# Kernel tuning notes

Hardware: AMD Instinct MI355X
Metric: run time of the kernel (lower is better)

## Reference

```python
import jax, jax.numpy as jnp
import numpy as np

B, N, K = 4, 4096, 10   # batch, num points, ED_nsample
SA, ED = 128, 4          # SA_conv_out, ED_conv_out


def _bn_pack(key, C):
    # rows: gamma, beta, running_mean, running_var (eval-mode BatchNorm1d)
    kg, kb, km, kv = jax.random.split(key, 4)
    g = 1.0 + 0.1 * jax.random.normal(kg, (C,))
    b = 0.1 * jax.random.normal(kb, (C,))
    m = 0.1 * jax.random.normal(km, (C,))
    v = jax.random.uniform(kv, (C,), minval=0.5, maxval=1.5)
    return jnp.stack([g, b, m, v])


def _conv_params(key, o, c):
    kw, kb = jax.random.split(key)
    return (jax.random.normal(kw, (o, c)) * (1.0 / np.sqrt(c)),
            0.01 * jax.random.normal(kb, (o,)))


def setup_inputs() -> dict:
    key = jax.random.key(0)
    ks = iter(jax.random.split(key, 32))
    inp = {}
    inp['pointcloud'] = jax.random.normal(next(ks), (B, N, 3), dtype=jnp.float32)
    inp['h1'] = jax.random.normal(next(ks), (B, SA, N), dtype=jnp.float32)      # Pointnet_Backbone output
    inp['h2'] = jax.random.normal(next(ks), (B, 1024, N), dtype=jnp.float32)    # DGCNN output
    shapes = {'dg1': (256, 1024), 'dg2': (64, 256), 'dg3': (32, 64),
              'c1': (512, 160), 'c2': (256, 512), 'c3': (128, 256), 'f': (128, 132)}
    for name, (o, c) in shapes.items():
        W, b = _conv_params(next(ks), o, c)
        inp['W_' + name], inp['b_' + name] = W, b
        inp['bn_' + name] = _bn_pack(next(ks), o)
    inp['W_ed1'] = jax.random.normal(next(ks), (ED, 3)) * 0.5
    inp['b_ed1'] = 0.01 * jax.random.normal(next(ks), (ED,))
    inp['W_ed2'] = jax.random.normal(next(ks), (ED, ED)) * 0.5
    inp['b_ed2'] = 0.01 * jax.random.normal(next(ks), (ED,))
    inp['numpoints'] = N
    return inp


def _bn1d(x, p, eps=1e-5):
    # x: [B, C, N]; p rows: gamma, beta, mean, var
    g, b, m, v = p
    inv = g * jax.lax.rsqrt(v + eps)
    return x * inv[:, None] + (b - m * inv)[:, None]


def _conv1(x, W, b):
    # 1x1 Conv1d == channel matmul. x: [B,C,N], W: [O,C]
    return jnp.einsum('oc,bcn->bon', W, x) + b[:, None]


def reference(pointcloud, h1, h2,
              W_dg1, b_dg1, bn_dg1, W_dg2, b_dg2, bn_dg2, W_dg3, b_dg3, bn_dg3,
              W_c1, b_c1, bn_c1, W_c2, b_c2, bn_c2, W_c3, b_c3, bn_c3,
              W_f, b_f, bn_f, W_ed1, b_ed1, W_ed2, b_ed2, numpoints):
    relu = jax.nn.relu
    xyz = pointcloud[..., :3]  # [B,N,3]

    # DGCNN feature reduction: 1024 -> 256 -> 64 -> 32
    h2_ = relu(_bn1d(_conv1(h2, W_dg1, b_dg1), bn_dg1))
    h2_ = relu(_bn1d(_conv1(h2_, W_dg2, b_dg2), bn_dg2))
    h2_ = relu(_bn1d(_conv1(h2_, W_dg3, b_dg3), bn_dg3))

    # fused feature: 160 -> 512 -> 256 -> 128
    f = jnp.concatenate([h1, h2_], axis=1)
    f_ = relu(_bn1d(_conv1(f, W_c1, b_c1), bn_c1))
    f_ = relu(_bn1d(_conv1(f_, W_c2, b_c2), bn_c2))
    f_ = relu(_bn1d(_conv1(f_, W_c3, b_c3), bn_c3))

    # knn_point: K nearest neighbors of each point within its cloud
    sq = jnp.sum(xyz * xyz, axis=-1)  # [B,N]
    d = sq[:, :, None] + sq[:, None, :] - 2.0 * jnp.einsum('bnd,bmd->bnm', xyz, xyz)
    _, idx = jax.lax.top_k(-d, K)  # [B,N,K]
    nbr = jax.vmap(lambda p, i: p[i])(xyz, idx)  # [B,N,K,3]

    # per-point 3x3 covariance + eigenvalues
    c = nbr - jnp.mean(nbr, axis=2, keepdims=True)
    cov = jnp.einsum('bnki,bnkj->bnij', c, c) / K  # [B,N,3,3]
    ev = jnp.linalg.eigvalsh(cov)  # [B,N,3] ascending

    # sub3_ED: Linear(3,4) -> ReLU -> Linear(4,4)
    ef = relu(ev @ W_ed1.T + b_ed1) @ W_ed2.T + b_ed2  # [B,N,4]
    ef_t = ef.transpose(0, 2, 1)  # [B,4,N]

    z = jnp.concatenate([f_, ef_t], axis=1)  # [B,132,N]
    z_ = relu(_bn1d(_conv1(z, W_f, b_f), bn_f))  # [B,128,N]
    return (xyz, z_, h1, h2_, ef_t)
```

## Files before the change

### kernel.cpp

```cpp
#include <hip/hip_runtime.h>
#include <hip/hip_bf16.h>
#include <math.h>

typedef __hip_bfloat16 bf16;

#define BB 4
#define NN 4096
#define KNB 10
#define KQ 8
#define KCAP 64

typedef __bf16 bfv8 __attribute__((ext_vector_type(8)));
typedef float  f32x4 __attribute__((ext_vector_type(4)));

__device__ __forceinline__ float ldT(const float* p) { return *p; }
__device__ __forceinline__ float ldT(const bf16* p)  { return __bfloat162float(*p); }
__device__ __forceinline__ void  stT(float* p, float v) { *p = v; }
__device__ __forceinline__ void  stT(bf16* p,  float v) { *p = __float2bfloat16(v); }

__device__ __forceinline__ unsigned short f2us(float x) {
  union { bf16 h; unsigned short u; } cv;
  cv.h = __float2bfloat16(x);
  return cv.u;
}

__device__ __forceinline__ void ld8bits(const float* p, unsigned short* s) {
  const float4 a = *(const float4*)p;
  const float4 b = *(const float4*)(p + 4);
  s[0] = f2us(a.x); s[1] = f2us(a.y); s[2] = f2us(a.z); s[3] = f2us(a.w);
  s[4] = f2us(b.x); s[5] = f2us(b.y); s[6] = f2us(b.z); s[7] = f2us(b.w);
}
__device__ __forceinline__ void ld8bits(const bf16* p, unsigned short* s) {
  const uint2 a = *(const uint2*)p;
  const uint2 b = *(const uint2*)(p + 4);
  s[0] = a.x & 0xffff; s[1] = a.x >> 16; s[2] = a.y & 0xffff; s[3] = a.y >> 16;
  s[4] = b.x & 0xffff; s[5] = b.x >> 16; s[6] = b.y & 0xffff; s[7] = b.y >> 16;
}

__device__ __forceinline__ bfv8 ldfrag(const unsigned short* p) {
  union { uint4 u; bfv8 v; } t;
  t.u = *(const uint4*)p;
  return t.v;
}

__global__ void k_sniff(const unsigned int* __restrict__ pcw, int* __restrict__ flag) {
  if (blockIdx.x == 0 && threadIdx.x == 0) {
    int hits = 0;
    for (int i = 0; i < 64; ++i) {
      unsigned int e = (pcw[i] >> 7) & 0xFF;
      if (e >= 100 && e <= 140) ++hits;
    }
    *flag = (hits >= 40) ? 1 : 0;
  }
}

template <class TI, class TO>
__global__ void k_prep(const int* __restrict__ flag, int want,
                       const TI* __restrict__ pc, float* __restrict__ xyz,
                       float4* __restrict__ pts4, TO* __restrict__ out0) {
  if (flag && *flag != want) return;
  int i = blockIdx.x * blockDim.x + threadIdx.x;
  if (i >= BB * NN) return;
  float x = ldT(pc + i * 3 + 0), y = ldT(pc + i * 3 + 1), z = ldT(pc + i * 3 + 2);
  xyz[i * 3 + 0] = x; xyz[i * 3 + 1] = y; xyz[i * 3 + 2] = z;
  const float nrm = fmaf(x, x, fmaf(y, y, z * z));
  pts4[i] = make_float4(x, y, z, nrm);
  stT(out0 + i * 3 + 0, x); stT(out0 + i * 3 + 1, y); stT(out0 + i * 3 + 2, z);
}

template <class TI, class TO>
__global__ void k_h1(const int* __restrict__ flag, int want,
                     const TI* __restrict__ h1, TO* __restrict__ out2,
                     bf16* __restrict__ fbuf) {
  if (flag && *flag != want) return;
  int i = blockIdx.x * blockDim.x + threadIdx.x;
  const int per = 128 * NN;
  if (i >= BB * per) return;
  float v = ldT(h1 + i);
  stT(out2 + i, v);
  int b = i / per, r = i - b * per;
  fbuf[(size_t)b * 160 * NN + r] = __float2bfloat16(v);
}

__global__ __launch_bounds__(256, 6) void k_knn(const float4* __restrict__ pts4,
                                                int* __restrict__ idxout) {
  __shared__ float smin[256][KQ + 1];
  __shared__ float stau[KQ];
  __shared__ float sd[KQ][KCAP];
  __shared__ int   si[KQ][KCAP];
  __shared__ unsigned int scnt[KQ];
  __shared__ float4 sq[KQ];
  const int tid = threadIdx.x;
  const int b = blockIdx.y;
  const int nBase = blockIdx.x * KQ;
  const float4* pb = pts4 + (size_t)b * NN;
  if (tid < KQ) { sq[tid] = pb[nBase + tid]; scnt[tid] = 0u; }
  __syncthreads();

  float qx[KQ], qy[KQ], qz[KQ], qn[KQ];
  #pragma unroll
  for (int q = 0; q < KQ; ++q) {
    const float4 p = sq[q];
    qx[q] = p.x; qy[q] = p.y; qz[q] = p.z; qn[q] = p.w;
  }

  float mv[KQ];
  #pragma unroll
  for (int q = 0; q < KQ; ++q) mv[q] = 1e30f;
  #pragma unroll 4
  for (int it = 0; it < 16; ++it) {
    const float4 c = pb[it * 256 + tid];
    #pragma unroll
    for (int q = 0; q < KQ; ++q) {
      const float dot = fmaf(qx[q], c.x, fmaf(qy[q], c.y, qz[q] * c.z));
      const float d = (qn[q] + c.w) - 2.0f * dot;
      mv[q] = fminf(mv[q], d);
    }
  }
  #pragma unroll
  for (int q = 0; q < KQ; ++q) smin[tid][q] = mv[q];
  __syncthreads();

  if (tid < KQ) {
    float arr[KNB];
    #pragma unroll
    for (int t = 0; t < KNB; ++t) arr[t] = 1e30f;
    for (int t = 0; t < 256; ++t) {
      const float v = smin[t][tid];
      if (v < arr[KNB - 1]) {
        arr[KNB - 1] = v;
        #pragma unroll
        for (int u = KNB - 1; u > 0; --u)
          if (arr[u] < arr[u - 1]) { const float tm = arr[u]; arr[u] = arr[u - 1]; arr[u - 1] = tm; }
      }
    }
    stau[tid] = arr[KNB - 1];
  }
  __syncthreads();
  float tq[KQ];
  #pragma unroll
  for (int q = 0; q < KQ; ++q) tq[q] = stau[q];

  #pragma unroll 4
  for (int it = 0; it < 16; ++it) {
    const float4 c = pb[it * 256 + tid];
    const int j = it * 256 + tid;
    #pragma unroll
    for (int q = 0; q < KQ; ++q) {
      const float dot = fmaf(qx[q], c.x, fmaf(qy[q], c.y, qz[q] * c.z));
      const float d = (qn[q] + c.w) - 2.0f * dot;
      if (d <= tq[q]) {
        const unsigned int pos = atomicAdd(&scnt[q], 1u);
        if (pos < KCAP) { sd[q][pos] = d; si[q][pos] = j; }
      }
    }
  }
  __syncthreads();

  if (tid < KQ) {
    const int qq = tid;
    const int nq = nBase + qq;
    int* op = idxout + ((size_t)b * NN + nq) * KNB;
    const unsigned int m = scnt[qq];
    float dk[KNB]; int ik[KNB];
    #pragma unroll
    for (int t = 0; t < KNB; ++t) { dk[t] = 1e30f; ik[t] = NN; }
    if (m <= KCAP) {
      for (unsigned int e = 0; e < m; ++e) {
        const float d = sd[qq][e];
        const int j = si[qq][e];
        if (d < dk[KNB - 1] || (d == dk[KNB - 1] && j < ik[KNB - 1])) {
          dk[KNB - 1] = d; ik[KNB - 1] = j;
          #pragma unroll
          for (int t = KNB - 1; t > 0; --t) {
            if (dk[t] < dk[t - 1] || (dk[t] == dk[t - 1] && ik[t] < ik[t - 1])) {
              const float td = dk[t]; dk[t] = dk[t - 1]; dk[t - 1] = td;
              const int ti = ik[t]; ik[t] = ik[t - 1]; ik[t - 1] = ti;
            }
          }
        }
      }
    } else {
      const float4 pQ = pb[nq];
      for (int j = 0; j < NN; ++j) {
        const float4 c = pb[j];
        const float dot = fmaf(pQ.x, c.x, fmaf(pQ.y, c.y, pQ.z * c.z));
        const float d = (pQ.w + c.w) - 2.0f * dot;
        if (d < dk[KNB - 1] || (d == dk[KNB - 1] && j < ik[KNB - 1])) {
          dk[KNB - 1] = d; ik[KNB - 1] = j;
          #pragma unroll
          for (int t = KNB - 1; t > 0; --t) {
            if (dk[t] < dk[t - 1] || (dk[t] == dk[t - 1] && ik[t] < ik[t - 1])) {
              const float td = dk[t]; dk[t] = dk[t - 1]; dk[t - 1] = td;
              const int ti = ik[t]; ik[t] = ik[t - 1]; ik[t - 1] = ti;
            }
          }
        }
      }
    }
    #pragma unroll
    for (int t = 0; t < KNB; ++t) op[t] = ik[t];
  }
}

template <class TP, class TO>
__global__ void k_ef(const int* __restrict__ flag, int want,
                     const float* __restrict__ xyz, const int* __restrict__ idxin,
                     const TP* __restrict__ W1, const TP* __restrict__ b1,
                     const TP* __restrict__ W2, const TP* __restrict__ b2,
                     TO* __restrict__ out4, bf16* __restrict__ zbuf) {
  if (flag && *flag != want) return;
  int i = blockIdx.x * blockDim.x + threadIdx.x;
  if (i >= BB * NN) return;
  int b = i / NN, n = i - b * NN;
  const float* xb = xyz + (size_t)b * NN * 3;
  const int* id = idxin + (size_t)i * KNB;
  double px[KNB], py[KNB], pz[KNB];
  double mx = 0, my = 0, mz = 0;
  #pragma unroll
  for (int k = 0; k < KNB; ++k) {
    int j = id[k];
    px[k] = (double)xb[j * 3 + 0];
    py[k] = (double)xb[j * 3 + 1];
    pz[k] = (double)xb[j * 3 + 2];
    mx += px[k]; my += py[k]; mz += pz[k];
  }
  mx /= KNB; my /= KNB; mz /= KNB;
  double c00 = 0, c01 = 0, c02 = 0, c11 = 0, c12 = 0, c22 = 0;
  #pragma unroll
  for (int k = 0; k < KNB; ++k) {
    double dx = px[k] - mx, dy = py[k] - my, dz = pz[k] - mz;
    c00 += dx * dx; c01 += dx * dy; c02 += dx * dz;
    c11 += dy * dy; c12 += dy * dz; c22 += dz * dz;
  }
  c00 /= KNB; c01 /= KNB; c02 /= KNB; c11 /= KNB; c12 /= KNB; c22 /= KNB;
  double e0, e1, e2;
  {
    double p1 = c01 * c01 + c02 * c02 + c12 * c12;
    double q = (c00 + c11 + c22) / 3.0;
    double d0 = c00 - q, d1 = c11 - q, d2 = c22 - q;
    double p2 = d0 * d0 + d1 * d1 + d2 * d2 + 2.0 * p1;
    if (p2 <= 0.0) {
      e0 = e1 = e2 = q;
    } else {
      double p = sqrt(p2 / 6.0);
      double ip = 1.0 / p;
      double b00 = d0 * ip, b11 = d1 * ip, b22 = d2 * ip;
      double b01 = c01 * ip, b02 = c02 * ip, b12 = c12 * ip;
      double det = b00 * (b11 * b22 - b12 * b12)
                 - b01 * (b01 * b22 - b12 * b02)
                 + b02 * (b01 * b12 - b11 * b02);
      double r = 0.5 * det;
      r = fmin(1.0, fmax(-1.0, r));
      double phi = acos(r) / 3.0;
      double lmax = q + 2.0 * p * cos(phi);
      double lmin = q + 2.0 * p * cos(phi + 2.0943951023931953);
      e0 = lmin; e2 = lmax; e1 = 3.0 * q - lmax - lmin;
    }
  }
  float ev0 = (float)e0, ev1 = (float)e1, ev2 = (float)e2;
  float h[4];
  #pragma unroll
  for (int o = 0; o < 4; ++o) {
    float t = ev0 * ldT(W1 + o * 3 + 0) + ev1 * ldT(W1 + o * 3 + 1)
            + ev2 * ldT(W1 + o * 3 + 2) + ldT(b1 + o);
    h[o] = fmaxf(t, 0.f);
  }
  #pragma unroll
  for (int j = 0; j < 4; ++j) {
    float t = h[0] * ldT(W2 + j * 4 + 0) + h[1] * ldT(W2 + j * 4 + 1)
            + h[2] * ldT(W2 + j * 4 + 2) + h[3] * ldT(W2 + j * 4 + 3)
            + ldT(b2 + j);
    stT(out4 + ((size_t)b * 4 + j) * NN + n, t);
    zbuf[((size_t)b * 132 + 128 + j) * NN + n] = __float2bfloat16(t);
  }
}

template <class TX, class TP, class TO>
__global__ __launch_bounds__(256) void k_gemm(
    const int* __restrict__ flag, int want,
    const TX* __restrict__ X, int C,
    const TP* __restrict__ W, const TP* __restrict__ bias,
    const TP* __restrict__ bn, int O,
    TO* __restrict__ Yout, int YRo, int yoffo,
    bf16* __restrict__ Ybuf, int YRb, int yoffb) {
  if (flag && *flag != want) return;
  __shared__ __align__(16) unsigned short Ws[64][72];
  __shared__ __align__(16) unsigned short Xs[64][72];
  const int tid  = threadIdx.x;
  const int lane = tid & 63;
  const int wv   = tid >> 6;
  const int wr = wv >> 1, wc = wv & 1;
  const int l15 = lane & 15, lg = lane >> 4;
  const int nBase = blockIdx.x * 64;
  const int oBase = blockIdx.y * 64;
  const int b = blockIdx.z;
  const TX* Xb = X + (size_t)b * C * NN;

  f32x4 acc[2][2];
  #pragma unroll
  for (int m = 0; m < 2; ++m)
    #pragma unroll
    for (int n = 0; n < 2; ++n) acc[m][n] = (f32x4){0.f, 0.f, 0.f, 0.f};

  const int wo  = tid >> 3;
  const int wc0 = (tid & 7) << 3;
  const int xc  = tid >> 3;
  const int xn0 = (tid & 7) << 3;

  for (int cb = 0; cb < C; cb += 64) {
    #pragma unroll
    for (int h = 0; h < 2; ++h) {
      const int o  = wo + h * 32;
      const int go = oBase + o, gc = cb + wc0;
      const int crem = C - gc;
      unsigned short s[8];
      if (go < O && crem >= 8) {
        ld8bits(W + (size_t)go * C + gc, s);
      } else {
        #pragma unroll
        for (int j = 0; j < 8; ++j)
          s[j] = (go < O && j < crem) ? f2us(ldT(W + (size_t)go * C + gc + j))
                                      : (unsigned short)0;
      }
      uint4 u;
      u.x = (unsigned)s[0] | ((unsigned)s[1] << 16);
      u.y = (unsigned)s[2] | ((unsigned)s[3] << 16);
      u.z = (unsigned)s[4] | ((unsigned)s[5] << 16);
      u.w = (unsigned)s[6] | ((unsigned)s[7] << 16);
      *(uint4*)&Ws[o][wc0] = u;
    }
    #pragma unroll
    for (int h = 0; h < 2; ++h) {
      const int c  = xc + h * 32;
      const int gc = cb + c;
      unsigned short s[8];
      if (gc < C) {
        ld8bits(Xb + (size_t)gc * NN + nBase + xn0, s);
      } else {
        #pragma unroll
        for (int j = 0; j < 8; ++j) s[j] = 0;
      }
      const int xcol = c ^ xn0;
      #pragma unroll
      for (int j = 0; j < 8; ++j) Xs[xn0 + j][xcol] = s[j];
    }
    __syncthreads();
    #pragma unroll
    for (int kk = 0; kk < 2; ++kk) {
      bfv8 af[2], xf[2];
      #pragma unroll
      for (int m = 0; m < 2; ++m)
        af[m] = ldfrag(&Ws[wr * 32 + m * 16 + l15][kk * 32 + lg * 8]);
      #pragma unroll
      for (int n = 0; n < 2; ++n) {
        const int nl  = wc * 32 + n * 16 + l15;
        const int col = (kk * 32 + lg * 8) ^ (((nl >> 3) & 7) << 3);
        xf[n] = ldfrag(&Xs[nl][col]);
      }
      #pragma unroll
      for (int m = 0; m < 2; ++m)
        #pragma unroll
        for (int n = 0; n < 2; ++n)
          acc[m][n] = __builtin_amdgcn_mfma_f32_16x16x32_bf16(af[m], xf[n], acc[m][n], 0, 0, 0);
    }
    __syncthreads();
  }

  #pragma unroll
  for (int m = 0; m < 2; ++m) {
    const int ob = oBase + wr * 32 + m * 16 + lg * 4;
    #pragma unroll
    for (int r = 0; r < 4; ++r) {
      const int oo = ob + r;
      if (oo >= O) continue;
      const float bc  = ldT(bias + oo);
      const float g   = ldT(bn + oo);
      const float bbv = ldT(bn + O + oo);
      const float mm  = ldT(bn + 2 * O + oo);
      const float vv  = ldT(bn + 3 * O + oo);
      const float inv = g / sqrtf(vv + 1e-5f);
      const float sh  = bbv - mm * inv;
      #pragma unroll
      for (int n = 0; n < 2; ++n) {
        const int nn2 = nBase + wc * 32 + n * 16 + l15;
        const float rv = fmaxf((acc[m][n][r] + bc) * inv + sh, 0.f);
        if (Yout) stT(Yout + ((size_t)b * YRo + yoffo + oo) * NN + nn2, rv);
        if (Ybuf) Ybuf[((size_t)b * YRb + yoffb + oo) * NN + nn2] = __float2bfloat16(rv);
      }
    }
  }
}

template <class TI>
static void launch_prep(int want, const int* flag, void* const* d_in, void* d_out,
                        hipStream_t stream, float* xyz, float4* pts4) {
  typedef TI TO;
  const TI* pc = (const TI*)d_in[0];
  TO* out0 = (TO*)d_out;
  k_prep<TI, TO><<<dim3((BB * NN + 255) / 256), 256, 0, stream>>>(flag, want, pc, xyz, pts4, out0);
}

template <class TI>
static void launch_rest(int want, const int* flag,
                        void* const* d_in, void* d_out, hipStream_t stream,
                        float* xyz, int* idx,
                        bf16* t512, bf16* t256, bf16* t64, bf16* fbuf, bf16* zbuf) {
  typedef TI TO;
  const TI* h1    = (const TI*)d_in[1];
  const TI* h2    = (const TI*)d_in[2];
  const TI* W_dg1 = (const TI*)d_in[3];  const TI* b_dg1 = (const TI*)d_in[4];  const TI* bn_dg1 = (const TI*)d_in[5];
  const TI* W_dg2 = (const TI*)d_in[6];  const TI* b_dg2 = (const TI*)d_in[7];  const TI* bn_dg2 = (const TI*)d_in[8];
  const TI* W_dg3 = (const TI*)d_in[9];  const TI* b_dg3 = (const TI*)d_in[10]; const TI* bn_dg3 = (const TI*)d_in[11];
  const TI* W_c1  = (const TI*)d_in[12]; const TI* b_c1  = (const TI*)d_in[13]; const TI* bn_c1  = (const TI*)d_in[14];
  const TI* W_c2  = (const TI*)d_in[15]; const TI* b_c2  = (const TI*)d_in[16]; const TI* bn_c2  = (const TI*)d_in[17];
  const TI* W_c3  = (const TI*)d_in[18]; const TI* b_c3  = (const TI*)d_in[19]; const TI* bn_c3  = (const TI*)d_in[20];
  const TI* W_f   = (const TI*)d_in[21]; const TI* b_f   = (const TI*)d_in[22]; const TI* bn_f   = (const TI*)d_in[23];
  const TI* W_ed1 = (const TI*)d_in[24]; const TI* b_ed1 = (const TI*)d_in[25];
  const TI* W_ed2 = (const TI*)d_in[26]; const TI* b_ed2 = (const TI*)d_in[27];

  TO* out  = (TO*)d_out;
  TO* out1 = out + 49152;
  TO* out2 = out1 + 2097152;
  TO* out3 = out2 + 2097152;
  TO* out4 = out3 + 524288;

  dim3 blk(256);
  k_h1<TI, TO><<<dim3((BB * 128 * NN + 255) / 256), 256, 0, stream>>>(flag, want, h1, out2, fbuf);
  k_gemm<TI, TI, TO><<<dim3(64, 4, BB), blk, 0, stream>>>(flag, want, h2, 1024, W_dg1, b_dg1, bn_dg1, 256,
                                                          (TO*)nullptr, 0, 0, t256, 256, 0);
  k_gemm<bf16, TI, TO><<<dim3(64, 1, BB), blk, 0, stream>>>(flag, want, t256, 256, W_dg2, b_dg2, bn_dg2, 64,
                                                            (TO*)nullptr, 0, 0, t64, 64, 0);
  k_gemm<bf16, TI, TO><<<dim3(64, 1, BB), blk, 0, stream>>>(flag, want, t64, 64, W_dg3, b_dg3, bn_dg3, 32,
                                                            out3, 32, 0, fbuf, 160, 128);
  k_gemm<bf16, TI, TO><<<dim3(64, 8, BB), blk, 0, stream>>>(flag, want, fbuf, 160, W_c1, b_c1, bn_c1, 512,
                                                            (TO*)nullptr, 0, 0, t512, 512, 0);
  k_ef<TI, TO><<<dim3((BB * NN + 255) / 256), 256, 0, stream>>>(flag, want, xyz, idx, W_ed1, b_ed1, W_ed2, b_ed2, out4, zbuf);
  k_gemm<bf16, TI, TO><<<dim3(64, 4, BB), blk, 0, stream>>>(flag, want, t512, 512, W_c2, b_c2, bn_c2, 256,
                                                            (TO*)nullptr, 0, 0, t256, 256, 0);
  k_gemm<bf16, TI, TO><<<dim3(64, 2, BB), blk, 0, stream>>>(flag, want, t256, 256, W_c3, b_c3, bn_c3, 128,
                                                            (TO*)nullptr, 0, 0, zbuf, 132, 0);
  k_gemm<bf16, TI, TO><<<dim3(64, 2, BB), blk, 0, stream>>>(flag, want, zbuf, 132, W_f, b_f, bn_f, 128,
                                                            out1, 128, 0, (bf16*)nullptr, 0, 0);
}

extern "C" void kernel_launch(void* const* d_in, const int* in_sizes, int n_in,
                              void* d_out, int out_size, void* d_ws, size_t ws_size,
                              hipStream_t stream) {
  char* ws = (char*)d_ws;
  int*    flag = (int*)(ws + 0);
  float*  xyz  = (float*)(ws + 1024);
  int*    idx  = (int*)(ws + 328704);
  bf16*   t512 = (bf16*)(ws + 1048576);
  bf16*   t256 = (bf16*)(ws + 17825792);
  bf16*   t64  = (bf16*)(ws + 26214400);
  bf16*   fbuf = (bf16*)(ws + 28311552);
  bf16*   zbuf = (bf16*)(ws + 33554432);
  float4* pts4 = (float4*)(ws + 1048576);

  int mode = -1;
  if (in_sizes) {
    if (in_sizes[0] == (int)(BB * NN * 3 * sizeof(float))) mode = 0;
    else if (in_sizes[0] == (int)(BB * NN * 3 * sizeof(bf16))) mode = 1;
  }

  if (mode < 0) {
    k_sniff<<<1, 64, 0, stream>>>((const unsigned int*)d_in[0], flag);
    launch_prep<float>(0, flag, d_in, d_out, stream, xyz, pts4);
    launch_prep<bf16>(1, flag, d_in, d_out, stream, xyz, pts4);
  } else if (mode == 0) {
    launch_prep<float>(0, nullptr, d_in, d_out, stream, xyz, pts4);
  } else {
    launch_prep<bf16>(1, nullptr, d_in, d_out, stream, xyz, pts4);
  }

  k_knn<<<dim3(NN / KQ, BB), 256, 0, stream>>>(pts4, idx);

  if (mode != 1) launch_rest<float>(0, mode < 0 ? flag : nullptr, d_in, d_out, stream,
                                    xyz, idx, t512, t256, t64, fbuf, zbuf);
  if (mode != 0) launch_rest<bf16>(1, mode < 0 ? flag : nullptr, d_in, d_out, stream,
                                   xyz, idx, t512, t256, t64, fbuf, zbuf);
}
```

Before: 409.6 us.

## Process 16 queries per KNN block with register prefetch of candidates

Doubles the number of query points handled per KNN block, so each candidate point load is reused across more distance computations and there are half as many blocks. Queries are loaded straight into registers instead of staged through shared memory, which drops one barrier. Both candidate scans are now fully unrolled with a one-step software prefetch. The cost is more registers per thread (launch bounds lowered to 4 waves), and the serial top-k selection done by the first KQ threads now covers 16 queries.

```diff
diff --git a/kernel.cpp b/kernel.cpp
--- a/kernel.cpp
+++ b/kernel.cpp
@@ -7,7 +7,7 @@
 #define BB 4
 #define NN 4096
 #define KNB 10
-#define KQ 8
+#define KQ 16
 #define KCAP 64
 
 typedef __bf16 bfv8 __attribute__((ext_vector_type(8)));
@@ -82,39 +82,44 @@
   fbuf[(size_t)b * 160 * NN + r] = __float2bfloat16(v);
 }
 
-__global__ __launch_bounds__(256, 6) void k_knn(const float4* __restrict__ pts4,
+__global__ __launch_bounds__(256, 4) void k_knn(const float4* __restrict__ pts4,
                                                 int* __restrict__ idxout) {
   __shared__ float smin[256][KQ + 1];
   __shared__ float stau[KQ];
   __shared__ float sd[KQ][KCAP];
   __shared__ int   si[KQ][KCAP];
   __shared__ unsigned int scnt[KQ];
-  __shared__ float4 sq[KQ];
   const int tid = threadIdx.x;
   const int b = blockIdx.y;
   const int nBase = blockIdx.x * KQ;
   const float4* pb = pts4 + (size_t)b * NN;
-  if (tid < KQ) { sq[tid] = pb[nBase + tid]; scnt[tid] = 0u; }
-  __syncthreads();
+  if (tid < KQ) scnt[tid] = 0u;
 
   float qx[KQ], qy[KQ], qz[KQ], qn[KQ];
   #pragma unroll
   for (int q = 0; q < KQ; ++q) {
-    const float4 p = sq[q];
+    const float4 p = pb[nBase + q];
     qx[q] = p.x; qy[q] = p.y; qz[q] = p.z; qn[q] = p.w;
   }
+  #pragma unroll
+  for (int q = 0; q < KQ; ++q)
+    asm volatile("" : "+v"(qx[q]), "+v"(qy[q]), "+v"(qz[q]), "+v"(qn[q]));
 
   float mv[KQ];
   #pragma unroll
   for (int q = 0; q < KQ; ++q) mv[q] = 1e30f;
-  #pragma unroll 4
-  for (int it = 0; it < 16; ++it) {
-    const float4 c = pb[it * 256 + tid];
-    #pragma unroll
-    for (int q = 0; q < KQ; ++q) {
-      const float dot = fmaf(qx[q], c.x, fmaf(qy[q], c.y, qz[q] * c.z));
-      const float d = (qn[q] + c.w) - 2.0f * dot;
-      mv[q] = fminf(mv[q], d);
+  {
+    float4 cA = pb[tid];
+    #pragma unroll
+    for (int it = 0; it < 16; ++it) {
+      const float4 cB = (it + 1 < 16) ? pb[(it + 1) * 256 + tid] : cA;
+      #pragma unroll
+      for (int q = 0; q < KQ; ++q) {
+        const float dot = fmaf(qx[q], cA.x, fmaf(qy[q], cA.y, qz[q] * cA.z));
+        const float d = (qn[q] + cA.w) - 2.0f * dot;
+        mv[q] = fminf(mv[q], d);
+      }
+      cA = cB;
     }
   }
   #pragma unroll
@@ -141,18 +146,22 @@
   #pragma unroll
   for (int q = 0; q < KQ; ++q) tq[q] = stau[q];
 
-  #pragma unroll 4
-  for (int it = 0; it < 16; ++it) {
-    const float4 c = pb[it * 256 + tid];
-    const int j = it * 256 + tid;
-    #pragma unroll
-    for (int q = 0; q < KQ; ++q) {
-      const float dot = fmaf(qx[q], c.x, fmaf(qy[q], c.y, qz[q] * c.z));
-      const float d = (qn[q] + c.w) - 2.0f * dot;
-      if (d <= tq[q]) {
-        const unsigned int pos = atomicAdd(&scnt[q], 1u);
-        if (pos < KCAP) { sd[q][pos] = d; si[q][pos] = j; }
-      }
+  {
+    float4 cA = pb[tid];
+    #pragma unroll
+    for (int it = 0; it < 16; ++it) {
+      const float4 cB = (it + 1 < 16) ? pb[(it + 1) * 256 + tid] : cA;
+      const int j = it * 256 + tid;
+      #pragma unroll
+      for (int q = 0; q < KQ; ++q) {
+        const float dot = fmaf(qx[q], cA.x, fmaf(qy[q], cA.y, qz[q] * cA.z));
+        const float d = (qn[q] + cA.w) - 2.0f * dot;
+        if (d <= tq[q]) {
+          const unsigned int pos = atomicAdd(&scnt[q], 1u);
+          if (pos < KCAP) { sd[q][pos] = d; si[q][pos] = j; }
+        }
+      }
+      cA = cB;
     }
   }
   __syncthreads();
```

Result: faster. 387.5 us (-5.4%).
